# Performance work log

Measured on AMD Instinct MI355X. Metric: run time of the kernel, lower is better.

The kernel has to match this reference:

```python
import jax, jax.numpy as jnp
import numpy as np

E, D, H, K, CH = 32, 512, 512, 4, 32  # n_sources, input_dim, hidden_dim, sparse_topk, confidence hidden
B = 2048
EPS = 1e-6

def setup_inputs() -> dict:
    key = jax.random.key(0)
    ks = jax.random.split(key, 8)
    init = lambda k, shape, fan_in: (jax.random.normal(k, shape, jnp.float32) / np.sqrt(fan_in)).astype(jnp.float32)
    return {
        "x":   jax.random.normal(ks[0], (B, D), jnp.float32),
        # per-expert transform MLPs (stacked over experts)
        "W1":  init(ks[1], (E, D, H), D), "b1": jnp.zeros((E, H), jnp.float32),
        "W2":  init(ks[2], (E, H, D), H), "b2": jnp.zeros((E, D), jnp.float32),
        # gating network
        "Wg1": init(ks[3], (D, H), D),    "bg1": jnp.zeros((H,), jnp.float32),
        "Wg2": init(ks[4], (H, E), H),    "bg2": jnp.zeros((E,), jnp.float32),
        # per-expert confidence nets
        "Wc1": init(ks[5], (E, D, CH), D), "bc1": jnp.zeros((E, CH), jnp.float32),
        "Wc2": init(ks[6], (E, CH, 1), CH), "bc2": jnp.zeros((E, 1), jnp.float32),
    }

def reference(x, W1, b1, W2, b2, Wg1, bg1, Wg2, bg2, Wc1, bc1, Wc2, bc2):
    # gate: softmax over experts, then top-k selection per token
    logits = jax.nn.relu(x @ Wg1 + bg1) @ Wg2 + bg2          # [B, E]
    weights = jax.nn.softmax(logits, axis=-1)                # [B, E]
    _, topi = jax.lax.top_k(weights, K)                      # [B, K] distinct expert ids

    # scan over experts, accumulating weighted-sum numerator and denominator.
    # out = sum_sel (w*c*o) / (sum_sel (w*c) + eps)  ==  torch's normalize-then-combine.
    def body(carry, packed):
        num, den = carry
        w1, bb1, w2, bb2, wc1, bbc1, wc2, bbc2, e = packed
        o = jax.nn.relu(x @ w1 + bb1) @ w2 + bb2             # [B, D] expert output
        c = jax.nn.sigmoid(jax.nn.relu(o @ wc1 + bbc1) @ wc2 + bbc2)[:, 0]  # [B]
        sel = jnp.any(topi == e, axis=1)                     # [B] token routed to expert e?
        cw = weights[:, e] * sel.astype(x.dtype) * c         # [B] gate-weight * confidence
        return (num + cw[:, None] * o, den + cw), None

    init = (jnp.zeros_like(x), jnp.zeros((x.shape[0],), x.dtype))
    (num, den), _ = jax.lax.scan(
        body, init,
        (W1, b1, W2, b2, Wc1, bc1, Wc2, bc2, jnp.arange(E, dtype=topi.dtype)))
    out = num / (den[:, None] + EPS)                         # [B, D]
    return out
```

## Files before the change

kernel.cpp:

```cpp
#include <hip/hip_runtime.h>
#include <hip/hip_bf16.h>

#define BT 2048
#define DD 512
#define HH 512
#define EE 32
#define KK 4
#define CHN 32
#define MAXCH 160

#define NB_CVT 512
#define NB_TRWC 272
#define NB_TRW 2112
#define NB_PREP (NB_CVT + NB_TRWC + NB_TRW)

typedef unsigned int u32;
typedef unsigned short u16;
typedef __attribute__((ext_vector_type(8))) short short8;
typedef __attribute__((ext_vector_type(4))) float f32x4;
typedef __attribute__((ext_vector_type(2))) u32 u32x2;
typedef __attribute__((ext_vector_type(4))) u32 u32x4;

__device__ inline u16 f2bf(float f) {
  u32 u = __builtin_bit_cast(u32, f);
  u32 r = (u + 0x7FFFu + ((u >> 16) & 1u)) >> 16;
  return (u16)r;
}
__device__ inline float bf16f(u16 b) {
  u32 u = ((u32)b) << 16;
  return __builtin_bit_cast(float, u);
}
__device__ inline u32 pack2bf(float a, float b) {
  return (u32)f2bf(a) | ((u32)f2bf(b) << 16);
}
__device__ inline void gload_lds16(const u32* g, u32* l) {
  __builtin_amdgcn_global_load_lds((const __attribute__((address_space(1))) u32*)g,
                                   (__attribute__((address_space(3))) u32*)l, 16, 0, 0);
}

__global__ __launch_bounds__(256)
void k_prep(const float* __restrict__ x, const float* __restrict__ W1,
            const float* __restrict__ W2, const float* __restrict__ Wc1,
            const float* __restrict__ Wg1, const float* __restrict__ Wg2,
            u16* __restrict__ xh, u16* __restrict__ xl,
            u32* __restrict__ img, u32* __restrict__ img_c) {
  const int bx = blockIdx.x;
  const int tid = threadIdx.x;
  if (bx < NB_CVT) {
    int gid = bx * 256 + tid;
    const float4* src = reinterpret_cast<const float4*>(x) + (size_t)gid * 2;
    float4 a = src[0], b = src[1];
    u32x4 hi = { pack2bf(a.x, a.y), pack2bf(a.z, a.w),
                 pack2bf(b.x, b.y), pack2bf(b.z, b.w) };
    float lx0 = a.x - bf16f(f2bf(a.x)), lx1 = a.y - bf16f(f2bf(a.y));
    float lx2 = a.z - bf16f(f2bf(a.z)), lx3 = a.w - bf16f(f2bf(a.w));
    float lx4 = b.x - bf16f(f2bf(b.x)), lx5 = b.y - bf16f(f2bf(b.y));
    float lx6 = b.z - bf16f(f2bf(b.z)), lx7 = b.w - bf16f(f2bf(b.w));
    u32x4 lo = { pack2bf(lx0, lx1), pack2bf(lx2, lx3),
                 pack2bf(lx4, lx5), pack2bf(lx6, lx7) };
    reinterpret_cast<u32x4*>(xh)[gid] = hi;
    reinterpret_cast<u32x4*>(xl)[gid] = lo;
  } else if (bx < NB_CVT + NB_TRWC) {
    int idx = (bx - NB_CVT) * 2 + (tid >> 7);
    int e = idx >> 4, s = idx & 15;
    int t127 = tid & 127;
    int q = t127 >> 5, col = t127 & 31;
    const float* W = (e < EE) ? (Wc1 + (size_t)e * DD * CHN) : Wg2;
    float v[8];
#pragma unroll
    for (int j = 0; j < 8; ++j)
      v[j] = W[(size_t)(s * 32 + q * 8 + j) * CHN + col];
    if (e == 33) {
#pragma unroll
      for (int j = 0; j < 8; ++j)
        v[j] = v[j] - bf16f(f2bf(v[j]));
    }
    u32x4 fr = { pack2bf(v[0], v[1]), pack2bf(v[2], v[3]),
                 pack2bf(v[4], v[5]), pack2bf(v[6], v[7]) };
    *reinterpret_cast<u32x4*>(img_c + ((size_t)e * 16 + s) * 512 + q * 128 + col * 4) = fr;
  } else {
    int u = bx - (NB_CVT + NB_TRWC);
    int z = u >> 5;
    int s = (u >> 1) & 15;
    int n = (u & 1) * 256 + tid;
    const float* W = (z < EE) ? (W1 + (size_t)z * DD * HH)
                   : (z < 2 * EE) ? (W2 + (size_t)(z - EE) * HH * DD)
                   : Wg1;
    float v[32];
#pragma unroll
    for (int k = 0; k < 32; k++)
      v[k] = W[(size_t)(s * 32 + k) * 512 + n];
    if (z == 65) {
#pragma unroll
      for (int k = 0; k < 32; k++)
        v[k] = v[k] - bf16f(f2bf(v[k]));
    }
    int nc = n >> 7, coll = n & 127;
    u32* ob = img + ((size_t)(z * 4 + nc) * 16 + s) * 2048 + coll * 4;
#pragma unroll
    for (int g = 0; g < 4; g++) {
      u32x4 fr = { pack2bf(v[g * 8 + 0], v[g * 8 + 1]),
                   pack2bf(v[g * 8 + 2], v[g * 8 + 3]),
                   pack2bf(v[g * 8 + 4], v[g * 8 + 5]),
                   pack2bf(v[g * 8 + 6], v[g * 8 + 7]) };
      *reinterpret_cast<u32x4*>(ob + g * 512) = fr;
    }
  }
}

__global__ __launch_bounds__(256)
void k_gate_mfma(const u16* __restrict__ xh, const u16* __restrict__ xl,
                 const u32* __restrict__ img, const float* __restrict__ bg1,
                 u16* __restrict__ hh, u16* __restrict__ hl) {
  __shared__ u32 stg[2][2][1024];
  const int chunk = blockIdx.x;
  const int hc = blockIdx.y;
  const int tid = threadIdx.x;
  const int w = tid >> 6, lane = tid & 63;
  const int l15 = lane & 15, q = lane >> 4;
  const int wm = w & 1, wn = w >> 1;
  const int nc = hc >> 1, co = (hc & 1) * 64;
  const u32* imgh = img + ((size_t)(64 * 4 + nc) * 16) * 2048;
  const u32* imgl = img + ((size_t)(65 * 4 + nc) * 16) * 2048;
  const int sq = tid >> 6, scol = tid & 63;
  auto stage = [&](int s, int b) {
    gload_lds16(imgh + s * 2048 + sq * 512 + (co + scol) * 4, stg[b][0] + tid * 4);
    gload_lds16(imgl + s * 2048 + sq * 512 + (co + scol) * 4, stg[b][1] + tid * 4);
  };
  const int t0 = chunk * 64 + wn * 32 + l15;
  const int t1 = t0 + 16;
  auto ldb = [&](const u16* src, int t, int s) {
    return *reinterpret_cast<const short8*>(src + (size_t)t * 512 + s * 32 + q * 8);
  };

  f32x4 acc[2][2];
#pragma unroll
  for (int a = 0; a < 2; a++)
#pragma unroll
    for (int b = 0; b < 2; b++) acc[a][b] = {0.f, 0.f, 0.f, 0.f};

  stage(0, 0);
  short8 bh[2], bl[2];
  bh[0] = ldb(xh, t0, 0); bh[1] = ldb(xh, t1, 0);
  bl[0] = ldb(xl, t0, 0); bl[1] = ldb(xl, t1, 0);
  __syncthreads();

  for (int s = 0; s < 16; ++s) {
    const u32* ch = stg[s & 1][0];
    const u32* cl = stg[s & 1][1];
    short8 nh[2], nl[2];
    if (s < 15) {
      stage(s + 1, (s + 1) & 1);
      nh[0] = ldb(xh, t0, s + 1); nh[1] = ldb(xh, t1, s + 1);
      nl[0] = ldb(xl, t0, s + 1); nl[1] = ldb(xl, t1, s + 1);
    }
#pragma unroll
    for (int mf = 0; mf < 2; ++mf) {
      int col = wm * 32 + mf * 16 + l15;
      short8 ah = *reinterpret_cast<const short8*>(ch + q * 256 + col * 4);
      short8 al = *reinterpret_cast<const short8*>(cl + q * 256 + col * 4);
#pragma unroll
      for (int nf = 0; nf < 2; ++nf) {
        acc[mf][nf] = __builtin_amdgcn_mfma_f32_16x16x32_bf16(ah, bh[nf], acc[mf][nf], 0, 0, 0);
        acc[mf][nf] = __builtin_amdgcn_mfma_f32_16x16x32_bf16(ah, bl[nf], acc[mf][nf], 0, 0, 0);
        acc[mf][nf] = __builtin_amdgcn_mfma_f32_16x16x32_bf16(al, bh[nf], acc[mf][nf], 0, 0, 0);
        acc[mf][nf] = __builtin_amdgcn_mfma_f32_16x16x32_bf16(al, bl[nf], acc[mf][nf], 0, 0, 0);
      }
    }
    __syncthreads();
    if (s < 15) {
      bh[0] = nh[0]; bh[1] = nh[1];
      bl[0] = nl[0]; bl[1] = nl[1];
    }
  }

#pragma unroll
  for (int mf = 0; mf < 2; ++mf) {
    int hcol = hc * 64 + wm * 32 + mf * 16 + q * 4;
    float4 bb = *reinterpret_cast<const float4*>(&bg1[hcol]);
#pragma unroll
    for (int nf = 0; nf < 2; ++nf) {
      int t = chunk * 64 + wn * 32 + nf * 16 + l15;
      float v0 = fmaxf(acc[mf][nf].x + bb.x, 0.f);
      float v1 = fmaxf(acc[mf][nf].y + bb.y, 0.f);
      float v2 = fmaxf(acc[mf][nf].z + bb.z, 0.f);
      float v3 = fmaxf(acc[mf][nf].w + bb.w, 0.f);
      u32x2 hi = { pack2bf(v0, v1), pack2bf(v2, v3) };
      float r0 = v0 - bf16f(f2bf(v0)), r1 = v1 - bf16f(f2bf(v1));
      float r2 = v2 - bf16f(f2bf(v2)), r3 = v3 - bf16f(f2bf(v3));
      u32x2 lo = { pack2bf(r0, r1), pack2bf(r2, r3) };
      *reinterpret_cast<u32x2*>(hh + (size_t)t * 512 + hcol) = hi;
      *reinterpret_cast<u32x2*>(hl + (size_t)t * 512 + hcol) = lo;
    }
  }
}

__global__ __launch_bounds__(256)
void k_route2(const u16* __restrict__ hh, const u16* __restrict__ hl,
              const u32* __restrict__ img_c, const float* __restrict__ bg2,
              float* __restrict__ wts, int* __restrict__ topi) {
  __shared__ u32 sh[8192];
  __shared__ u32 sl_[8192];
  const int chunk = blockIdx.x;
  const int tid = threadIdx.x;
  const int w = tid >> 6, lane = tid & 63;
  const int l15 = lane & 15, q = lane >> 4;
  const u32* srch = img_c + (size_t)32 * 16 * 512;
  const u32* srcl = img_c + (size_t)33 * 16 * 512;
#pragma unroll
  for (int i = 0; i < 8; ++i) {
    gload_lds16(srch + tid * 4 + i * 1024, sh + tid * 4 + i * 1024);
    gload_lds16(srcl + tid * 4 + i * 1024, sl_ + tid * 4 + i * 1024);
  }
  __syncthreads();

  const int t = chunk * 64 + w * 16 + l15;
  const u16* rh = hh + (size_t)t * 512;
  const u16* rl = hl + (size_t)t * 512;
  f32x4 acc0 = {0.f, 0.f, 0.f, 0.f}, acc1 = {0.f, 0.f, 0.f, 0.f};
#pragma unroll
  for (int st = 0; st < 16; ++st) {
    short8 bh = *reinterpret_cast<const short8*>(rh + st * 32 + q * 8);
    short8 bl = *reinterpret_cast<const short8*>(rl + st * 32 + q * 8);
    short8 ah0 = *reinterpret_cast<const short8*>(sh + st * 512 + q * 128 + l15 * 4);
    short8 ah1 = *reinterpret_cast<const short8*>(sh + st * 512 + q * 128 + (16 + l15) * 4);
    short8 al0 = *reinterpret_cast<const short8*>(sl_ + st * 512 + q * 128 + l15 * 4);
    short8 al1 = *reinterpret_cast<const short8*>(sl_ + st * 512 + q * 128 + (16 + l15) * 4);
    acc0 = __builtin_amdgcn_mfma_f32_16x16x32_bf16(ah0, bh, acc0, 0, 0, 0);
    acc0 = __builtin_amdgcn_mfma_f32_16x16x32_bf16(ah0, bl, acc0, 0, 0, 0);
    acc0 = __builtin_amdgcn_mfma_f32_16x16x32_bf16(al0, bh, acc0, 0, 0, 0);
    acc0 = __builtin_amdgcn_mfma_f32_16x16x32_bf16(al0, bl, acc0, 0, 0, 0);
    acc1 = __builtin_amdgcn_mfma_f32_16x16x32_bf16(ah1, bh, acc1, 0, 0, 0);
    acc1 = __builtin_amdgcn_mfma_f32_16x16x32_bf16(ah1, bl, acc1, 0, 0, 0);
    acc1 = __builtin_amdgcn_mfma_f32_16x16x32_bf16(al1, bh, acc1, 0, 0, 0);
    acc1 = __builtin_amdgcn_mfma_f32_16x16x32_bf16(al1, bl, acc1, 0, 0, 0);
  }

  float lv[8];
  int li[8];
#pragma unroll
  for (int i = 0; i < 4; ++i) {
    li[i] = q * 4 + i;
    lv[i] = acc0[i] + bg2[li[i]];
    li[4 + i] = 16 + q * 4 + i;
    lv[4 + i] = acc1[i] + bg2[li[4 + i]];
  }
  float mx = lv[0];
#pragma unroll
  for (int k = 1; k < 8; ++k) mx = fmaxf(mx, lv[k]);
  mx = fmaxf(mx, __shfl_xor(mx, 16));
  mx = fmaxf(mx, __shfl_xor(mx, 32));
  float ex[8], sm = 0.f;
#pragma unroll
  for (int k = 0; k < 8; ++k) { ex[k] = expf(lv[k] - mx); sm += ex[k]; }
  sm += __shfl_xor(sm, 16);
  sm += __shfl_xor(sm, 32);
  float inv = 1.f / sm;
  float4 w0 = { ex[0] * inv, ex[1] * inv, ex[2] * inv, ex[3] * inv };
  float4 w1 = { ex[4] * inv, ex[5] * inv, ex[6] * inv, ex[7] * inv };
  *reinterpret_cast<float4*>(&wts[(size_t)t * EE + q * 4]) = w0;
  *reinterpret_cast<float4*>(&wts[(size_t)t * EE + 16 + q * 4]) = w1;
  unsigned used = 0;
  for (int j = 0; j < KK; ++j) {
    float bv = -1e30f;
    int bi = 64;
#pragma unroll
    for (int k = 0; k < 8; ++k) {
      if (!((used >> k) & 1u) && (lv[k] > bv || (lv[k] == bv && li[k] < bi))) {
        bv = lv[k]; bi = li[k];
      }
    }
#pragma unroll
    for (int m = 16; m <= 32; m <<= 1) {
      float ov = __shfl_xor(bv, m);
      int oi = __shfl_xor(bi, m);
      if (ov > bv || (ov == bv && oi < bi)) { bv = ov; bi = oi; }
    }
    if (q == 0) topi[(t << 2) | j] = bi;
#pragma unroll
    for (int k = 0; k < 8; ++k)
      if (li[k] == bi) used |= 1u << k;
  }
}

__global__ __launch_bounds__(1024)
void k_build(const int* __restrict__ topi, int* __restrict__ cnt,
             int* __restrict__ tlist, int* __restrict__ chunk2e,
             int* __restrict__ chunkloc) {
  __shared__ int lcnt[EE];
  const int tid = threadIdx.x;
  if (tid < EE) lcnt[tid] = 0;
  __syncthreads();
  for (int i = tid; i < BT * KK; i += 1024) {
    int e = topi[i];
    int pos = atomicAdd(&lcnt[e], 1);
    tlist[(size_t)e * BT + pos] = i;
  }
  __syncthreads();
  if (tid < EE) {
    int e = tid;
    cnt[e] = lcnt[e];
    int off = 0, tot = 0;
    for (int j = 0; j < EE; ++j) {
      int nj = (lcnt[j] + 63) >> 6;
      if (j < e) off += nj;
      tot += nj;
    }
    int myn = (lcnt[e] + 63) >> 6;
    for (int j = 0; j < myn; ++j) {
      chunk2e[off + j] = e; chunkloc[off + j] = j;
    }
    for (int idx = tot + e; idx < MAXCH; idx += EE) {
      chunk2e[idx] = -1; chunkloc[idx] = 0;
    }
  }
}

__device__ inline int remap_chunk(int bx) {
  return (bx & 7) * (MAXCH / 8) + (bx >> 3);
}

__global__ __launch_bounds__(256)
void k_gemm1(const u16* __restrict__ xb, const u32* __restrict__ img,
             const float* __restrict__ b1, const int* __restrict__ cnt,
             const int* __restrict__ tlist, const int* __restrict__ chunk2e,
             const int* __restrict__ chunkloc, u32* __restrict__ hid) {
  __shared__ u32 stg[2][4096];
  __shared__ int tkl[64];
  const int c = remap_chunk(blockIdx.x);
  const int e = chunk2e[c];
  if (e < 0) return;
  const int hc = blockIdx.y;
  const int loc = chunkloc[c];
  const int nt = cnt[e];
  const int tid = threadIdx.x;
  const int w = tid >> 6, lane = tid & 63;
  const int l15 = lane & 15, q = lane >> 4;
  const int wm = w & 1, wn = w >> 1;

  const u32* imgb = img + ((size_t)(e * 4 + hc) * 16) * 2048;
  auto stage = [&](int st, u32* dst) {
    const u32* src = imgb + st * 4096;
#pragma unroll
    for (int i = 0; i < 4; i++)
      gload_lds16(src + tid * 4 + i * 1024, dst + tid * 4 + i * 1024);
  };

  stage(0, stg[0]);
  if (tid < 64) {
    int i = min(loc * 64 + tid, nt - 1);
    tkl[tid] = tlist[(size_t)e * BT + i] >> 2;
  }
  __syncthreads();

  const int t0 = tkl[wn * 32 + l15];
  const int t1 = tkl[wn * 32 + 16 + l15];
  auto ldb = [&](int t, int st, int ss) {
    return *reinterpret_cast<const short8*>(
        xb + (size_t)t * 512 + st * 64 + ss * 32 + q * 8);
  };

  f32x4 acc[4][2];
#pragma unroll
  for (int a = 0; a < 4; a++)
#pragma unroll
    for (int b = 0; b < 2; b++) acc[a][b] = {0.f, 0.f, 0.f, 0.f};

  short8 bfr[2][2];
  bfr[0][0] = ldb(t0, 0, 0); bfr[0][1] = ldb(t0, 0, 1);
  bfr[1][0] = ldb(t1, 0, 0); bfr[1][1] = ldb(t1, 0, 1);

  for (int st = 0; st < 8; ++st) {
    const u32* cur = stg[st & 1];
    short8 nb[2][2];
    if (st < 7) {
      stage(st + 1, stg[(st + 1) & 1]);
      nb[0][0] = ldb(t0, st + 1, 0); nb[0][1] = ldb(t0, st + 1, 1);
      nb[1][0] = ldb(t1, st + 1, 0); nb[1][1] = ldb(t1, st + 1, 1);
    }
#pragma unroll
    for (int ss = 0; ss < 2; ++ss) {
#pragma unroll
      for (int mf = 0; mf < 4; ++mf) {
        int col = wm * 64 + mf * 16 + l15;
        short8 af = *reinterpret_cast<const short8*>(
            cur + ss * 2048 + q * 512 + col * 4);
        acc[mf][0] = __builtin_amdgcn_mfma_f32_16x16x32_bf16(af, bfr[0][ss], acc[mf][0], 0, 0, 0);
        acc[mf][1] = __builtin_amdgcn_mfma_f32_16x16x32_bf16(af, bfr[1][ss], acc[mf][1], 0, 0, 0);
      }
    }
    __syncthreads();
    if (st < 7) {
      bfr[0][0] = nb[0][0]; bfr[0][1] = nb[0][1];
      bfr[1][0] = nb[1][0]; bfr[1][1] = nb[1][1];
    }
  }

  const float* b1e = b1 + (size_t)e * HH;
#pragma unroll
  for (int mf = 0; mf < 4; ++mf) {
    int h0 = hc * 128 + wm * 64 + mf * 16 + q * 4;
    float4 bb = *reinterpret_cast<const float4*>(b1e + h0);
#pragma unroll
    for (int nf = 0; nf < 2; ++nf) {
      int local = wn * 32 + nf * 16 + l15;
      int prow = c * 64 + local;
      float v0 = fmaxf(acc[mf][nf].x + bb.x, 0.f);
      float v1 = fmaxf(acc[mf][nf].y + bb.y, 0.f);
      float v2 = fmaxf(acc[mf][nf].z + bb.z, 0.f);
      float v3 = fmaxf(acc[mf][nf].w + bb.w, 0.f);
      u32x2 pk = { pack2bf(v0, v1), pack2bf(v2, v3) };
      *reinterpret_cast<u32x2*>(hid + (size_t)prow * 256 + (h0 >> 1)) = pk;
    }
  }
}

__global__ __launch_bounds__(256)
void k_gemm2(const u32* __restrict__ hid, const u32* __restrict__ img,
             const float* __restrict__ b2, const int* __restrict__ cnt,
             const int* __restrict__ tlist, const int* __restrict__ chunk2e,
             const int* __restrict__ chunkloc, u16* __restrict__ o_p) {
  __shared__ u32 stg[2][4096];
  __shared__ int tke[64];
  const int c = remap_chunk(blockIdx.x);
  const int e = chunk2e[c];
  if (e < 0) return;
  const int dc = blockIdx.y;
  const int loc = chunkloc[c];
  const int nt = cnt[e];
  const int tid = threadIdx.x;
  const int w = tid >> 6, lane = tid & 63;
  const int l15 = lane & 15, q = lane >> 4;
  const int wm = w & 1, wn = w >> 1;
  const int rows_c = min(64, nt - loc * 64);

  const u32* imgb = img + ((size_t)((EE + e) * 4 + dc) * 16) * 2048;
  auto stage = [&](int st, u32* dst) {
    const u32* src = imgb + st * 4096;
#pragma unroll
    for (int i = 0; i < 4; i++)
      gload_lds16(src + tid * 4 + i * 1024, dst + tid * 4 + i * 1024);
  };

  stage(0, stg[0]);
  if (tid < 64) {
    int i = min(loc * 64 + tid, nt - 1);
    tke[tid] = tlist[(size_t)e * BT + i];
  }
  __syncthreads();

  const u16* hid16 = (const u16*)hid;
  const int pr0 = c * 64 + wn * 32 + l15;
  const int pr1 = pr0 + 16;
  auto ldb = [&](int pr, int st, int ss) {
    return *reinterpret_cast<const short8*>(
        hid16 + (size_t)pr * 512 + st * 64 + ss * 32 + q * 8);
  };

  f32x4 acc[4][2];
#pragma unroll
  for (int a = 0; a < 4; a++)
#pragma unroll
    for (int b = 0; b < 2; b++) acc[a][b] = {0.f, 0.f, 0.f, 0.f};

  short8 bfr[2][2];
  bfr[0][0] = ldb(pr0, 0, 0); bfr[0][1] = ldb(pr0, 0, 1);
  bfr[1][0] = ldb(pr1, 0, 0); bfr[1][1] = ldb(pr1, 0, 1);

  for (int st = 0; st < 8; ++st) {
    const u32* cur = stg[st & 1];
    short8 nb[2][2];
    if (st < 7) {
      stage(st + 1, stg[(st + 1) & 1]);
      nb[0][0] = ldb(pr0, st + 1, 0); nb[0][1] = ldb(pr0, st + 1, 1);
      nb[1][0] = ldb(pr1, st + 1, 0); nb[1][1] = ldb(pr1, st + 1, 1);
    }
#pragma unroll
    for (int ss = 0; ss < 2; ++ss) {
#pragma unroll
      for (int mf = 0; mf < 4; ++mf) {
        int col = wm * 64 + mf * 16 + l15;
        short8 af = *reinterpret_cast<const short8*>(
            cur + ss * 2048 + q * 512 + col * 4);
        acc[mf][0] = __builtin_amdgcn_mfma_f32_16x16x32_bf16(af, bfr[0][ss], acc[mf][0], 0, 0, 0);
        acc[mf][1] = __builtin_amdgcn_mfma_f32_16x16x32_bf16(af, bfr[1][ss], acc[mf][1], 0, 0, 0);
      }
    }
    __syncthreads();
    if (st < 7) {
      bfr[0][0] = nb[0][0]; bfr[0][1] = nb[0][1];
      bfr[1][0] = nb[1][0]; bfr[1][1] = nb[1][1];
    }
  }

  const float* b2e = b2 + (size_t)e * DD;
#pragma unroll
  for (int mf = 0; mf < 4; ++mf) {
    int d0 = dc * 128 + wm * 64 + mf * 16 + q * 4;
    float4 bb = *reinterpret_cast<const float4*>(b2e + d0);
#pragma unroll
    for (int nf = 0; nf < 2; ++nf) {
      int local = wn * 32 + nf * 16 + l15;
      if (local < rows_c) {
        int ent = tke[local];
        u32x2 pk = { pack2bf(acc[mf][nf].x + bb.x, acc[mf][nf].y + bb.y),
                     pack2bf(acc[mf][nf].z + bb.z, acc[mf][nf].w + bb.w) };
        *reinterpret_cast<u32x2*>(&o_p[(size_t)ent * DD + d0]) = pk;
      }
    }
  }
}

__global__ __launch_bounds__(256)
void k_conf2(const u16* __restrict__ o_p, const u32* __restrict__ img_c,
             const float* __restrict__ bc1, const float* __restrict__ Wc2,
             const float* __restrict__ bc2, const float* __restrict__ wts,
             const int* __restrict__ cnt, const int* __restrict__ tlist,
             const int* __restrict__ chunk2e, const int* __restrict__ chunkloc,
             float* __restrict__ cw) {
  __shared__ u32 stg[8192];
  __shared__ int tke[64];
  const int c = remap_chunk(blockIdx.x);
  const int e = chunk2e[c];
  if (e < 0) return;
  const int loc = chunkloc[c];
  const int nt = cnt[e];
  const int tid = threadIdx.x;
  const int w = tid >> 6, lane = tid & 63;
  const int l15 = lane & 15, q = lane >> 4;

  const u32* src = img_c + (size_t)e * 16 * 512;
#pragma unroll
  for (int i = 0; i < 8; ++i)
    gload_lds16(src + tid * 4 + i * 1024, stg + tid * 4 + i * 1024);
  if (tid < 64) {
    int i = min(loc * 64 + tid, nt - 1);
    tke[tid] = tlist[(size_t)e * BT + i];
  }
  __syncthreads();

  const int rows_c = min(64, nt - loc * 64);
  const int local = w * 16 + l15;
  const int ent = tke[local];
  const u16* orow = o_p + (size_t)ent * DD;

  f32x4 acc0 = {0.f, 0.f, 0.f, 0.f}, acc1 = {0.f, 0.f, 0.f, 0.f};
#pragma unroll
  for (int st = 0; st < 16; ++st) {
    short8 bfrag = *reinterpret_cast<const short8*>(orow + st * 32 + q * 8);
    short8 af0 = *reinterpret_cast<const short8*>(
        stg + st * 512 + q * 128 + l15 * 4);
    short8 af1 = *reinterpret_cast<const short8*>(
        stg + st * 512 + q * 128 + (16 + l15) * 4);
    acc0 = __builtin_amdgcn_mfma_f32_16x16x32_bf16(af0, bfrag, acc0, 0, 0, 0);
    acc1 = __builtin_amdgcn_mfma_f32_16x16x32_bf16(af1, bfrag, acc1, 0, 0, 0);
  }

  float part = 0.f;
#pragma unroll
  for (int i = 0; i < 4; ++i) {
    int ch0 = q * 4 + i, ch1 = 16 + q * 4 + i;
    float h0 = fmaxf(acc0[i] + bc1[(size_t)e * CHN + ch0], 0.f);
    float h1 = fmaxf(acc1[i] + bc1[(size_t)e * CHN + ch1], 0.f);
    part = fmaf(h0, Wc2[(size_t)e * CHN + ch0], part);
    part = fmaf(h1, Wc2[(size_t)e * CHN + ch1], part);
  }
  part += __shfl_xor(part, 16);
  part += __shfl_xor(part, 32);
  if (q == 0 && local < rows_c) {
    float cv = 1.f / (1.f + expf(-(part + bc2[e])));
    cw[ent] = wts[(size_t)(ent >> 2) * EE + e] * cv;
  }
}

__global__ __launch_bounds__(256)
void k_combine(const u16* __restrict__ o_p, const float* __restrict__ cw,
               float* __restrict__ out) {
  int gid = blockIdx.x * 256 + threadIdx.x;
  int t = gid >> 6;
  int j = gid & 63;
  float c0 = cw[t * 4 + 0], c1 = cw[t * 4 + 1];
  float c2 = cw[t * 4 + 2], c3 = cw[t * 4 + 3];
  float den = c0 + c1 + c2 + c3 + 1e-6f;
  const u16* base = o_p + (size_t)t * 4 * DD + j * 8;
  short8 v0 = *reinterpret_cast<const short8*>(base + 0 * DD);
  short8 v1 = *reinterpret_cast<const short8*>(base + 1 * DD);
  short8 v2 = *reinterpret_cast<const short8*>(base + 2 * DD);
  short8 v3 = *reinterpret_cast<const short8*>(base + 3 * DD);
  float r[8];
#pragma unroll
  for (int i = 0; i < 8; ++i) {
    r[i] = (c0 * bf16f((u16)v0[i]) + c1 * bf16f((u16)v1[i]) +
            c2 * bf16f((u16)v2[i]) + c3 * bf16f((u16)v3[i])) / den;
  }
  float4 o0 = { r[0], r[1], r[2], r[3] };
  float4 o1 = { r[4], r[5], r[6], r[7] };
  float4* dst = reinterpret_cast<float4*>(out + (size_t)t * DD + j * 8);
  dst[0] = o0;
  dst[1] = o1;
}

extern "C" void kernel_launch(void* const* d_in, const int* in_sizes, int n_in,
                              void* d_out, int out_size, void* d_ws, size_t ws_size,
                              hipStream_t stream) {
  const float* x   = (const float*)d_in[0];
  const float* W1  = (const float*)d_in[1];
  const float* b1  = (const float*)d_in[2];
  const float* W2  = (const float*)d_in[3];
  const float* b2  = (const float*)d_in[4];
  const float* Wg1 = (const float*)d_in[5];
  const float* bg1 = (const float*)d_in[6];
  const float* Wg2 = (const float*)d_in[7];
  const float* bg2 = (const float*)d_in[8];
  const float* Wc1 = (const float*)d_in[9];
  const float* bc1 = (const float*)d_in[10];
  const float* Wc2 = (const float*)d_in[11];
  const float* bc2 = (const float*)d_in[12];
  float* out = (float*)d_out;

  char* p = (char*)d_ws;
  u16* xh = (u16*)p;            p += (size_t)BT * DD * 2;
  u32* img = (u32*)p;           p += (size_t)66 * 4 * 16 * 2048 * 4;
  u16* hh = (u16*)p;
  u16* hl = (u16*)(p + (size_t)2 * 1024 * 1024);
  u16* xl = (u16*)(p + (size_t)4 * 1024 * 1024);
  u32* hid = (u32*)p;           p += (size_t)MAXCH * 64 * DD * 2;
  float* wts = (float*)p;       p += (size_t)BT * EE * 4;
  float* cw  = (float*)p;       p += (size_t)BT * KK * 4;
  u16* o_p = (u16*)p;           p += (size_t)BT * KK * DD * 2;
  int* cnt = (int*)p;           p += 256;
  int* tlist = (int*)p;         p += (size_t)EE * BT * 4;
  int* chunk2e = (int*)p;       p += 1024;
  int* chunkloc = (int*)p;      p += 1024;
  u32* img_c = (u32*)p;         p += (size_t)34 * 16 * 512 * 4;
  int* topi = (int*)p;          p += (size_t)BT * KK * 4;

  k_prep<<<NB_PREP, 256, 0, stream>>>(x, W1, W2, Wc1, Wg1, Wg2,
                                      xh, xl, img, img_c);
  k_gate_mfma<<<dim3(32, 8), 256, 0, stream>>>(xh, xl, img, bg1, hh, hl);
  k_route2<<<32, 256, 0, stream>>>(hh, hl, img_c, bg2, wts, topi);
  k_build<<<1, 1024, 0, stream>>>(topi, cnt, tlist, chunk2e, chunkloc);
  k_gemm1<<<dim3(MAXCH, 4), 256, 0, stream>>>(xh, img, b1, cnt, tlist,
                                              chunk2e, chunkloc, hid);
  k_gemm2<<<dim3(MAXCH, 4), 256, 0, stream>>>(hid, img, b2, cnt, tlist,
                                              chunk2e, chunkloc, o_p);
  k_conf2<<<MAXCH, 256, 0, stream>>>(o_p, img_c, bc1, Wc2, bc2, wts,
                                     cnt, tlist, chunk2e, chunkloc, cw);
  k_combine<<<(BT * (DD / 8)) / 256, 256, 0, stream>>>(o_p, cw, out);
}
```

Measured before the change: 103.3 us.

## Fuse gate, route and build kernels, and conf into gemm2, via last-block atomics

Merges the gate GEMM, the routing softmax/top-k and the expert list build into one kernel. The last block to finish each token chunk does the routing, and the last block overall builds the per-expert token lists, both detected with atomic counters and thread fences. In the same way, the confidence net is folded into gemm2: the last of the four column blocks per chunk computes it. This removes three kernel launches and their inter-kernel gaps, at the cost of serialized tail work in single blocks, an extra memset of the flag counters, and a larger shared-memory footprint.

```diff
diff --git a/kernel.cpp b/kernel.cpp
--- a/kernel.cpp
+++ b/kernel.cpp
@@ -109,209 +109,220 @@
 }
 
 __global__ __launch_bounds__(256)
-void k_gate_mfma(const u16* __restrict__ xh, const u16* __restrict__ xl,
-                 const u32* __restrict__ img, const float* __restrict__ bg1,
-                 u16* __restrict__ hh, u16* __restrict__ hl) {
-  __shared__ u32 stg[2][2][1024];
+void k_gate_fused(const u16* __restrict__ xh, const u16* __restrict__ xl,
+                  const u32* __restrict__ img, const float* __restrict__ bg1,
+                  const u32* __restrict__ img_c, const float* __restrict__ bg2,
+                  u16* __restrict__ hh, u16* __restrict__ hl,
+                  float* __restrict__ wts, int* __restrict__ topi,
+                  int* __restrict__ done1, int* __restrict__ gdone,
+                  int* __restrict__ cnt, int* __restrict__ tlist,
+                  int* __restrict__ chunk2e, int* __restrict__ chunkloc) {
+  __shared__ u32 smem[16384];
+  __shared__ int winflag, bwin;
   const int chunk = blockIdx.x;
   const int hc = blockIdx.y;
   const int tid = threadIdx.x;
   const int w = tid >> 6, lane = tid & 63;
   const int l15 = lane & 15, q = lane >> 4;
   const int wm = w & 1, wn = w >> 1;
-  const int nc = hc >> 1, co = (hc & 1) * 64;
-  const u32* imgh = img + ((size_t)(64 * 4 + nc) * 16) * 2048;
-  const u32* imgl = img + ((size_t)(65 * 4 + nc) * 16) * 2048;
-  const int sq = tid >> 6, scol = tid & 63;
-  auto stage = [&](int s, int b) {
-    gload_lds16(imgh + s * 2048 + sq * 512 + (co + scol) * 4, stg[b][0] + tid * 4);
-    gload_lds16(imgl + s * 2048 + sq * 512 + (co + scol) * 4, stg[b][1] + tid * 4);
-  };
-  const int t0 = chunk * 64 + wn * 32 + l15;
-  const int t1 = t0 + 16;
-  auto ldb = [&](const u16* src, int t, int s) {
-    return *reinterpret_cast<const short8*>(src + (size_t)t * 512 + s * 32 + q * 8);
-  };
-
-  f32x4 acc[2][2];
-#pragma unroll
-  for (int a = 0; a < 2; a++)
-#pragma unroll
-    for (int b = 0; b < 2; b++) acc[a][b] = {0.f, 0.f, 0.f, 0.f};
-
-  stage(0, 0);
-  short8 bh[2], bl[2];
-  bh[0] = ldb(xh, t0, 0); bh[1] = ldb(xh, t1, 0);
-  bl[0] = ldb(xl, t0, 0); bl[1] = ldb(xl, t1, 0);
+
+  {
+    auto S = [&](int b, int h2) { return smem + (b * 2 + h2) * 1024; };
+    const int nc = hc >> 1, co = (hc & 1) * 64;
+    const u32* imgh = img + ((size_t)(64 * 4 + nc) * 16) * 2048;
+    const u32* imgl = img + ((size_t)(65 * 4 + nc) * 16) * 2048;
+    const int sq = tid >> 6, scol = tid & 63;
+    auto stage = [&](int s, int b) {
+      gload_lds16(imgh + s * 2048 + sq * 512 + (co + scol) * 4, S(b, 0) + tid * 4);
+      gload_lds16(imgl + s * 2048 + sq * 512 + (co + scol) * 4, S(b, 1) + tid * 4);
+    };
+    const int t0 = chunk * 64 + wn * 32 + l15;
+    const int t1 = t0 + 16;
+    auto ldb = [&](const u16* src, int t, int s) {
+      return *reinterpret_cast<const short8*>(src + (size_t)t * 512 + s * 32 + q * 8);
+    };
+
+    f32x4 acc[2][2];
+#pragma unroll
+    for (int a = 0; a < 2; a++)
+#pragma unroll
+      for (int b = 0; b < 2; b++) acc[a][b] = {0.f, 0.f, 0.f, 0.f};
+
+    stage(0, 0);
+    short8 bh[2], bl[2];
+    bh[0] = ldb(xh, t0, 0); bh[1] = ldb(xh, t1, 0);
+    bl[0] = ldb(xl, t0, 0); bl[1] = ldb(xl, t1, 0);
+    __syncthreads();
+
+    for (int s = 0; s < 16; ++s) {
+      const u32* ch = S(s & 1, 0);
+      const u32* cl = S(s & 1, 1);
+      short8 nh[2], nl[2];
+      if (s < 15) {
+        stage(s + 1, (s + 1) & 1);
+        nh[0] = ldb(xh, t0, s + 1); nh[1] = ldb(xh, t1, s + 1);
+        nl[0] = ldb(xl, t0, s + 1); nl[1] = ldb(xl, t1, s + 1);
+      }
+#pragma unroll
+      for (int mf = 0; mf < 2; ++mf) {
+        int col = wm * 32 + mf * 16 + l15;
+        short8 ah = *reinterpret_cast<const short8*>(ch + q * 256 + col * 4);
+        short8 al = *reinterpret_cast<const short8*>(cl + q * 256 + col * 4);
+#pragma unroll
+        for (int nf = 0; nf < 2; ++nf) {
+          acc[mf][nf] = __builtin_amdgcn_mfma_f32_16x16x32_bf16(ah, bh[nf], acc[mf][nf], 0, 0, 0);
+          acc[mf][nf] = __builtin_amdgcn_mfma_f32_16x16x32_bf16(ah, bl[nf], acc[mf][nf], 0, 0, 0);
+          acc[mf][nf] = __builtin_amdgcn_mfma_f32_16x16x32_bf16(al, bh[nf], acc[mf][nf], 0, 0, 0);
+          acc[mf][nf] = __builtin_amdgcn_mfma_f32_16x16x32_bf16(al, bl[nf], acc[mf][nf], 0, 0, 0);
+        }
+      }
+      __syncthreads();
+      if (s < 15) {
+        bh[0] = nh[0]; bh[1] = nh[1];
+        bl[0] = nl[0]; bl[1] = nl[1];
+      }
+    }
+
+#pragma unroll
+    for (int mf = 0; mf < 2; ++mf) {
+      int hcol = hc * 64 + wm * 32 + mf * 16 + q * 4;
+      float4 bb = *reinterpret_cast<const float4*>(&bg1[hcol]);
+#pragma unroll
+      for (int nf = 0; nf < 2; ++nf) {
+        int t = chunk * 64 + wn * 32 + nf * 16 + l15;
+        float v0 = fmaxf(acc[mf][nf].x + bb.x, 0.f);
+        float v1 = fmaxf(acc[mf][nf].y + bb.y, 0.f);
+        float v2 = fmaxf(acc[mf][nf].z + bb.z, 0.f);
+        float v3 = fmaxf(acc[mf][nf].w + bb.w, 0.f);
+        u32x2 hi = { pack2bf(v0, v1), pack2bf(v2, v3) };
+        float r0 = v0 - bf16f(f2bf(v0)), r1 = v1 - bf16f(f2bf(v1));
+        float r2 = v2 - bf16f(f2bf(v2)), r3 = v3 - bf16f(f2bf(v3));
+        u32x2 lo = { pack2bf(r0, r1), pack2bf(r2, r3) };
+        *reinterpret_cast<u32x2*>(hh + (size_t)t * 512 + hcol) = hi;
+        *reinterpret_cast<u32x2*>(hl + (size_t)t * 512 + hcol) = lo;
+      }
+    }
+  }
+
+  __threadfence();
+  if (tid == 0) winflag = (atomicAdd(&done1[chunk], 1) == 7);
   __syncthreads();
-
-  for (int s = 0; s < 16; ++s) {
-    const u32* ch = stg[s & 1][0];
-    const u32* cl = stg[s & 1][1];
-    short8 nh[2], nl[2];
-    if (s < 15) {
-      stage(s + 1, (s + 1) & 1);
-      nh[0] = ldb(xh, t0, s + 1); nh[1] = ldb(xh, t1, s + 1);
-      nl[0] = ldb(xl, t0, s + 1); nl[1] = ldb(xl, t1, s + 1);
-    }
-#pragma unroll
-    for (int mf = 0; mf < 2; ++mf) {
-      int col = wm * 32 + mf * 16 + l15;
-      short8 ah = *reinterpret_cast<const short8*>(ch + q * 256 + col * 4);
-      short8 al = *reinterpret_cast<const short8*>(cl + q * 256 + col * 4);
-#pragma unroll
-      for (int nf = 0; nf < 2; ++nf) {
-        acc[mf][nf] = __builtin_amdgcn_mfma_f32_16x16x32_bf16(ah, bh[nf], acc[mf][nf], 0, 0, 0);
-        acc[mf][nf] = __builtin_amdgcn_mfma_f32_16x16x32_bf16(ah, bl[nf], acc[mf][nf], 0, 0, 0);
-        acc[mf][nf] = __builtin_amdgcn_mfma_f32_16x16x32_bf16(al, bh[nf], acc[mf][nf], 0, 0, 0);
-        acc[mf][nf] = __builtin_amdgcn_mfma_f32_16x16x32_bf16(al, bl[nf], acc[mf][nf], 0, 0, 0);
-      }
+  if (!winflag) return;
+  __threadfence();
+
+  {
+    u32* sh = smem;
+    u32* sl_ = smem + 8192;
+    const u32* srch = img_c + (size_t)32 * 16 * 512;
+    const u32* srcl = img_c + (size_t)33 * 16 * 512;
+#pragma unroll
+    for (int i = 0; i < 8; ++i) {
+      gload_lds16(srch + tid * 4 + i * 1024, sh + tid * 4 + i * 1024);
+      gload_lds16(srcl + tid * 4 + i * 1024, sl_ + tid * 4 + i * 1024);
     }
     __syncthreads();
-    if (s < 15) {
-      bh[0] = nh[0]; bh[1] = nh[1];
-      bl[0] = nl[0]; bl[1] = nl[1];
-    }
-  }
-
-#pragma unroll
-  for (int mf = 0; mf < 2; ++mf) {
-    int hcol = hc * 64 + wm * 32 + mf * 16 + q * 4;
-    float4 bb = *reinterpret_cast<const float4*>(&bg1[hcol]);
-#pragma unroll
-    for (int nf = 0; nf < 2; ++nf) {
-      int t = chunk * 64 + wn * 32 + nf * 16 + l15;
-      float v0 = fmaxf(acc[mf][nf].x + bb.x, 0.f);
-      float v1 = fmaxf(acc[mf][nf].y + bb.y, 0.f);
-      float v2 = fmaxf(acc[mf][nf].z + bb.z, 0.f);
-      float v3 = fmaxf(acc[mf][nf].w + bb.w, 0.f);
-      u32x2 hi = { pack2bf(v0, v1), pack2bf(v2, v3) };
-      float r0 = v0 - bf16f(f2bf(v0)), r1 = v1 - bf16f(f2bf(v1));
-      float r2 = v2 - bf16f(f2bf(v2)), r3 = v3 - bf16f(f2bf(v3));
-      u32x2 lo = { pack2bf(r0, r1), pack2bf(r2, r3) };
-      *reinterpret_cast<u32x2*>(hh + (size_t)t * 512 + hcol) = hi;
-      *reinterpret_cast<u32x2*>(hl + (size_t)t * 512 + hcol) = lo;
-    }
-  }
-}
-
-__global__ __launch_bounds__(256)
-void k_route2(const u16* __restrict__ hh, const u16* __restrict__ hl,
-              const u32* __restrict__ img_c, const float* __restrict__ bg2,
-              float* __restrict__ wts, int* __restrict__ topi) {
-  __shared__ u32 sh[8192];
-  __shared__ u32 sl_[8192];
-  const int chunk = blockIdx.x;
-  const int tid = threadIdx.x;
-  const int w = tid >> 6, lane = tid & 63;
-  const int l15 = lane & 15, q = lane >> 4;
-  const u32* srch = img_c + (size_t)32 * 16 * 512;
-  const u32* srcl = img_c + (size_t)33 * 16 * 512;
-#pragma unroll
-  for (int i = 0; i < 8; ++i) {
-    gload_lds16(srch + tid * 4 + i * 1024, sh + tid * 4 + i * 1024);
-    gload_lds16(srcl + tid * 4 + i * 1024, sl_ + tid * 4 + i * 1024);
-  }
+
+    const int t = chunk * 64 + w * 16 + l15;
+    const u16* rh = hh + (size_t)t * 512;
+    const u16* rl = hl + (size_t)t * 512;
+    f32x4 acc0 = {0.f, 0.f, 0.f, 0.f}, acc1 = {0.f, 0.f, 0.f, 0.f};
+#pragma unroll
+    for (int st = 0; st < 16; ++st) {
+      short8 bh = *reinterpret_cast<const short8*>(rh + st * 32 + q * 8);
+      short8 bl = *reinterpret_cast<const short8*>(rl + st * 32 + q * 8);
+      short8 ah0 = *reinterpret_cast<const short8*>(sh + st * 512 + q * 128 + l15 * 4);
+      short8 ah1 = *reinterpret_cast<const short8*>(sh + st * 512 + q * 128 + (16 + l15) * 4);
+      short8 al0 = *reinterpret_cast<const short8*>(sl_ + st * 512 + q * 128 + l15 * 4);
+      short8 al1 = *reinterpret_cast<const short8*>(sl_ + st * 512 + q * 128 + (16 + l15) * 4);
+      acc0 = __builtin_amdgcn_mfma_f32_16x16x32_bf16(ah0, bh, acc0, 0, 0, 0);
+      acc0 = __builtin_amdgcn_mfma_f32_16x16x32_bf16(ah0, bl, acc0, 0, 0, 0);
+      acc0 = __builtin_amdgcn_mfma_f32_16x16x32_bf16(al0, bh, acc0, 0, 0, 0);
+      acc0 = __builtin_amdgcn_mfma_f32_16x16x32_bf16(al0, bl, acc0, 0, 0, 0);
+      acc1 = __builtin_amdgcn_mfma_f32_16x16x32_bf16(ah1, bh, acc1, 0, 0, 0);
+      acc1 = __builtin_amdgcn_mfma_f32_16x16x32_bf16(ah1, bl, acc1, 0, 0, 0);
+      acc1 = __builtin_amdgcn_mfma_f32_16x16x32_bf16(al1, bh, acc1, 0, 0, 0);
+      acc1 = __builtin_amdgcn_mfma_f32_16x16x32_bf16(al1, bl, acc1, 0, 0, 0);
+    }
+
+    float lv[8];
+    int li[8];
+#pragma unroll
+    for (int i = 0; i < 4; ++i) {
+      li[i] = q * 4 + i;
+      lv[i] = acc0[i] + bg2[li[i]];
+      li[4 + i] = 16 + q * 4 + i;
+      lv[4 + i] = acc1[i] + bg2[li[4 + i]];
+    }
+    float mx = lv[0];
+#pragma unroll
+    for (int k = 1; k < 8; ++k) mx = fmaxf(mx, lv[k]);
+    mx = fmaxf(mx, __shfl_xor(mx, 16));
+    mx = fmaxf(mx, __shfl_xor(mx, 32));
+    float ex[8], sm = 0.f;
+#pragma unroll
+    for (int k = 0; k < 8; ++k) { ex[k] = expf(lv[k] - mx); sm += ex[k]; }
+    sm += __shfl_xor(sm, 16);
+    sm += __shfl_xor(sm, 32);
+    float inv = 1.f / sm;
+    float4 w0 = { ex[0] * inv, ex[1] * inv, ex[2] * inv, ex[3] * inv };
+    float4 w1 = { ex[4] * inv, ex[5] * inv, ex[6] * inv, ex[7] * inv };
+    *reinterpret_cast<float4*>(&wts[(size_t)t * EE + q * 4]) = w0;
+    *reinterpret_cast<float4*>(&wts[(size_t)t * EE + 16 + q * 4]) = w1;
+    unsigned used = 0;
+    for (int j = 0; j < KK; ++j) {
+      float bv = -1e30f;
+      int bi = 64;
+#pragma unroll
+      for (int k = 0; k < 8; ++k) {
+        if (!((used >> k) & 1u) && (lv[k] > bv || (lv[k] == bv && li[k] < bi))) {
+          bv = lv[k]; bi = li[k];
+        }
+      }
+#pragma unroll
+      for (int m = 16; m <= 32; m <<= 1) {
+        float ov = __shfl_xor(bv, m);
+        int oi = __shfl_xor(bi, m);
+        if (ov > bv || (ov == bv && oi < bi)) { bv = ov; bi = oi; }
+      }
+      if (q == 0) topi[(t << 2) | j] = bi;
+#pragma unroll
+      for (int k = 0; k < 8; ++k)
+        if (li[k] == bi) used |= 1u << k;
+    }
+  }
+
+  __threadfence();
+  if (tid == 0) bwin = (atomicAdd(gdone, 1) == 31);
   __syncthreads();
-
-  const int t = chunk * 64 + w * 16 + l15;
-  const u16* rh = hh + (size_t)t * 512;
-  const u16* rl = hl + (size_t)t * 512;
-  f32x4 acc0 = {0.f, 0.f, 0.f, 0.f}, acc1 = {0.f, 0.f, 0.f, 0.f};
-#pragma unroll
-  for (int st = 0; st < 16; ++st) {
-    short8 bh = *reinterpret_cast<const short8*>(rh + st * 32 + q * 8);
-    short8 bl = *reinterpret_cast<const short8*>(rl + st * 32 + q * 8);
-    short8 ah0 = *reinterpret_cast<const short8*>(sh + st * 512 + q * 128 + l15 * 4);
-    short8 ah1 = *reinterpret_cast<const short8*>(sh + st * 512 + q * 128 + (16 + l15) * 4);
-    short8 al0 = *reinterpret_cast<const short8*>(sl_ + st * 512 + q * 128 + l15 * 4);
-    short8 al1 = *reinterpret_cast<const short8*>(sl_ + st * 512 + q * 128 + (16 + l15) * 4);
-    acc0 = __builtin_amdgcn_mfma_f32_16x16x32_bf16(ah0, bh, acc0, 0, 0, 0);
-    acc0 = __builtin_amdgcn_mfma_f32_16x16x32_bf16(ah0, bl, acc0, 0, 0, 0);
-    acc0 = __builtin_amdgcn_mfma_f32_16x16x32_bf16(al0, bh, acc0, 0, 0, 0);
-    acc0 = __builtin_amdgcn_mfma_f32_16x16x32_bf16(al0, bl, acc0, 0, 0, 0);
-    acc1 = __builtin_amdgcn_mfma_f32_16x16x32_bf16(ah1, bh, acc1, 0, 0, 0);
-    acc1 = __builtin_amdgcn_mfma_f32_16x16x32_bf16(ah1, bl, acc1, 0, 0, 0);
-    acc1 = __builtin_amdgcn_mfma_f32_16x16x32_bf16(al1, bh, acc1, 0, 0, 0);
-    acc1 = __builtin_amdgcn_mfma_f32_16x16x32_bf16(al1, bl, acc1, 0, 0, 0);
-  }
-
-  float lv[8];
-  int li[8];
-#pragma unroll
-  for (int i = 0; i < 4; ++i) {
-    li[i] = q * 4 + i;
-    lv[i] = acc0[i] + bg2[li[i]];
-    li[4 + i] = 16 + q * 4 + i;
-    lv[4 + i] = acc1[i] + bg2[li[4 + i]];
-  }
-  float mx = lv[0];
-#pragma unroll
-  for (int k = 1; k < 8; ++k) mx = fmaxf(mx, lv[k]);
-  mx = fmaxf(mx, __shfl_xor(mx, 16));
-  mx = fmaxf(mx, __shfl_xor(mx, 32));
-  float ex[8], sm = 0.f;
-#pragma unroll
-  for (int k = 0; k < 8; ++k) { ex[k] = expf(lv[k] - mx); sm += ex[k]; }
-  sm += __shfl_xor(sm, 16);
-  sm += __shfl_xor(sm, 32);
-  float inv = 1.f / sm;
-  float4 w0 = { ex[0] * inv, ex[1] * inv, ex[2] * inv, ex[3] * inv };
-  float4 w1 = { ex[4] * inv, ex[5] * inv, ex[6] * inv, ex[7] * inv };
-  *reinterpret_cast<float4*>(&wts[(size_t)t * EE + q * 4]) = w0;
-  *reinterpret_cast<float4*>(&wts[(size_t)t * EE + 16 + q * 4]) = w1;
-  unsigned used = 0;
-  for (int j = 0; j < KK; ++j) {
-    float bv = -1e30f;
-    int bi = 64;
-#pragma unroll
-    for (int k = 0; k < 8; ++k) {
-      if (!((used >> k) & 1u) && (lv[k] > bv || (lv[k] == bv && li[k] < bi))) {
-        bv = lv[k]; bi = li[k];
-      }
-    }
-#pragma unroll
-    for (int m = 16; m <= 32; m <<= 1) {
-      float ov = __shfl_xor(bv, m);
-      int oi = __shfl_xor(bi, m);
-      if (ov > bv || (ov == bv && oi < bi)) { bv = ov; bi = oi; }
-    }
-    if (q == 0) topi[(t << 2) | j] = bi;
-#pragma unroll
-    for (int k = 0; k < 8; ++k)
-      if (li[k] == bi) used |= 1u << k;
-  }
-}
-
-__global__ __launch_bounds__(1024)
-void k_build(const int* __restrict__ topi, int* __restrict__ cnt,
-             int* __restrict__ tlist, int* __restrict__ chunk2e,
-             int* __restrict__ chunkloc) {
-  __shared__ int lcnt[EE];
-  const int tid = threadIdx.x;
-  if (tid < EE) lcnt[tid] = 0;
-  __syncthreads();
-  for (int i = tid; i < BT * KK; i += 1024) {
-    int e = topi[i];
-    int pos = atomicAdd(&lcnt[e], 1);
-    tlist[(size_t)e * BT + pos] = i;
-  }
-  __syncthreads();
-  if (tid < EE) {
-    int e = tid;
-    cnt[e] = lcnt[e];
-    int off = 0, tot = 0;
-    for (int j = 0; j < EE; ++j) {
-      int nj = (lcnt[j] + 63) >> 6;
-      if (j < e) off += nj;
-      tot += nj;
-    }
-    int myn = (lcnt[e] + 63) >> 6;
-    for (int j = 0; j < myn; ++j) {
-      chunk2e[off + j] = e; chunkloc[off + j] = j;
-    }
-    for (int idx = tot + e; idx < MAXCH; idx += EE) {
-      chunk2e[idx] = -1; chunkloc[idx] = 0;
+  if (!bwin) return;
+  __threadfence();
+
+  {
+    int* lcnt = (int*)smem;
+    if (tid < EE) lcnt[tid] = 0;
+    __syncthreads();
+    for (int i = tid; i < BT * KK; i += 256) {
+      int e2 = topi[i];
+      int pos = atomicAdd(&lcnt[e2], 1);
+      tlist[(size_t)e2 * BT + pos] = i;
+    }
+    __syncthreads();
+    if (tid < EE) {
+      int e2 = tid;
+      cnt[e2] = lcnt[e2];
+      int off = 0, tot = 0;
+      for (int j = 0; j < EE; ++j) {
+        int nj = (lcnt[j] + 63) >> 6;
+        if (j < e2) off += nj;
+        tot += nj;
+      }
+      int myn = (lcnt[e2] + 63) >> 6;
+      for (int j = 0; j < myn; ++j) {
+        chunk2e[off + j] = e2; chunkloc[off + j] = j;
+      }
+      for (int idx = tot + e2; idx < MAXCH; idx += EE) {
+        chunk2e[idx] = -1; chunkloc[idx] = 0;
+      }
     }
   }
 }
@@ -416,12 +427,17 @@
 }
 
 __global__ __launch_bounds__(256)
-void k_gemm2(const u32* __restrict__ hid, const u32* __restrict__ img,
-             const float* __restrict__ b2, const int* __restrict__ cnt,
-             const int* __restrict__ tlist, const int* __restrict__ chunk2e,
-             const int* __restrict__ chunkloc, u16* __restrict__ o_p) {
+void k_gemm2c(const u32* __restrict__ hid, const u32* __restrict__ img,
+              const float* __restrict__ b2, const int* __restrict__ cnt,
+              const int* __restrict__ tlist, const int* __restrict__ chunk2e,
+              const int* __restrict__ chunkloc, u16* __restrict__ o_p,
+              const u32* __restrict__ img_c, const float* __restrict__ bc1,
+              const float* __restrict__ Wc2, const float* __restrict__ bc2,
+              const float* __restrict__ wts, int* __restrict__ done2,
+              float* __restrict__ cw) {
   __shared__ u32 stg[2][4096];
   __shared__ int tke[64];
+  __shared__ int cwin;
   const int c = remap_chunk(blockIdx.x);
   const int e = chunk2e[c];
   if (e < 0) return;
@@ -509,67 +525,52 @@
       }
     }
   }
-}
-
-__global__ __launch_bounds__(256)
-void k_conf2(const u16* __restrict__ o_p, const u32* __restrict__ img_c,
-             const float* __restrict__ bc1, const float* __restrict__ Wc2,
-             const float* __restrict__ bc2, const float* __restrict__ wts,
-             const int* __restrict__ cnt, const int* __restrict__ tlist,
-             const int* __restrict__ chunk2e, const int* __restrict__ chunkloc,
-             float* __restrict__ cw) {
-  __shared__ u32 stg[8192];
-  __shared__ int tke[64];
-  const int c = remap_chunk(blockIdx.x);
-  const int e = chunk2e[c];
-  if (e < 0) return;
-  const int loc = chunkloc[c];
-  const int nt = cnt[e];
-  const int tid = threadIdx.x;
-  const int w = tid >> 6, lane = tid & 63;
-  const int l15 = lane & 15, q = lane >> 4;
-
-  const u32* src = img_c + (size_t)e * 16 * 512;
-#pragma unroll
-  for (int i = 0; i < 8; ++i)
-    gload_lds16(src + tid * 4 + i * 1024, stg + tid * 4 + i * 1024);
-  if (tid < 64) {
-    int i = min(loc * 64 + tid, nt - 1);
-    tke[tid] = tlist[(size_t)e * BT + i];
-  }
+
+  __threadfence();
+  if (tid == 0) cwin = (atomicAdd(&done2[c], 1) == 3);
   __syncthreads();
-
-  const int rows_c = min(64, nt - loc * 64);
-  const int local = w * 16 + l15;
-  const int ent = tke[local];
-  const u16* orow = o_p + (size_t)ent * DD;
-
-  f32x4 acc0 = {0.f, 0.f, 0.f, 0.f}, acc1 = {0.f, 0.f, 0.f, 0.f};
-#pragma unroll
-  for (int st = 0; st < 16; ++st) {
-    short8 bfrag = *reinterpret_cast<const short8*>(orow + st * 32 + q * 8);
-    short8 af0 = *reinterpret_cast<const short8*>(
-        stg + st * 512 + q * 128 + l15 * 4);
-    short8 af1 = *reinterpret_cast<const short8*>(
-        stg + st * 512 + q * 128 + (16 + l15) * 4);
-    acc0 = __builtin_amdgcn_mfma_f32_16x16x32_bf16(af0, bfrag, acc0, 0, 0, 0);
-    acc1 = __builtin_amdgcn_mfma_f32_16x16x32_bf16(af1, bfrag, acc1, 0, 0, 0);
-  }
-
-  float part = 0.f;
-#pragma unroll
-  for (int i = 0; i < 4; ++i) {
-    int ch0 = q * 4 + i, ch1 = 16 + q * 4 + i;
-    float h0 = fmaxf(acc0[i] + bc1[(size_t)e * CHN + ch0], 0.f);
-    float h1 = fmaxf(acc1[i] + bc1[(size_t)e * CHN + ch1], 0.f);
-    part = fmaf(h0, Wc2[(size_t)e * CHN + ch0], part);
-    part = fmaf(h1, Wc2[(size_t)e * CHN + ch1], part);
-  }
-  part += __shfl_xor(part, 16);
-  part += __shfl_xor(part, 32);
-  if (q == 0 && local < rows_c) {
-    float cv = 1.f / (1.f + expf(-(part + bc2[e])));
-    cw[ent] = wts[(size_t)(ent >> 2) * EE + e] * cv;
+  if (!cwin) return;
+  __threadfence();
+
+  {
+    u32* cs = &stg[0][0];
+    const u32* src = img_c + (size_t)e * 16 * 512;
+#pragma unroll
+    for (int i = 0; i < 8; ++i)
+      gload_lds16(src + tid * 4 + i * 1024, cs + tid * 4 + i * 1024);
+    __syncthreads();
+
+    const int local = w * 16 + l15;
+    const int ent = tke[local];
+    const u16* orow = o_p + (size_t)ent * DD;
+
+    f32x4 acc0 = {0.f, 0.f, 0.f, 0.f}, acc1 = {0.f, 0.f, 0.f, 0.f};
+#pragma unroll
+    for (int st = 0; st < 16; ++st) {
+      short8 bfrag = *reinterpret_cast<const short8*>(orow + st * 32 + q * 8);
+      short8 af0 = *reinterpret_cast<const short8*>(
+          cs + st * 512 + q * 128 + l15 * 4);
+      short8 af1 = *reinterpret_cast<const short8*>(
+          cs + st * 512 + q * 128 + (16 + l15) * 4);
+      acc0 = __builtin_amdgcn_mfma_f32_16x16x32_bf16(af0, bfrag, acc0, 0, 0, 0);
+      acc1 = __builtin_amdgcn_mfma_f32_16x16x32_bf16(af1, bfrag, acc1, 0, 0, 0);
+    }
+
+    float part = 0.f;
+#pragma unroll
+    for (int i = 0; i < 4; ++i) {
+      int ch0 = q * 4 + i, ch1 = 16 + q * 4 + i;
+      float h0 = fmaxf(acc0[i] + bc1[(size_t)e * CHN + ch0], 0.f);
+      float h1 = fmaxf(acc1[i] + bc1[(size_t)e * CHN + ch1], 0.f);
+      part = fmaf(h0, Wc2[(size_t)e * CHN + ch0], part);
+      part = fmaf(h1, Wc2[(size_t)e * CHN + ch1], part);
+    }
+    part += __shfl_xor(part, 16);
+    part += __shfl_xor(part, 32);
+    if (q == 0 && local < rows_c) {
+      float cv = 1.f / (1.f + expf(-(part + bc2[e])));
+      cw[ent] = wts[(size_t)(ent >> 2) * EE + e] * cv;
+    }
   }
 }
 
@@ -634,17 +635,22 @@
   int* chunkloc = (int*)p;      p += 1024;
   u32* img_c = (u32*)p;         p += (size_t)34 * 16 * 512 * 4;
   int* topi = (int*)p;          p += (size_t)BT * KK * 4;
-
+  int* flags = (int*)p;         p += 1024;
+  int* done1 = flags;
+  int* gdone = flags + 32;
+  int* done2 = flags + 33;
+
+  hipMemsetAsync(flags, 0, 1024, stream);
   k_prep<<<NB_PREP, 256, 0, stream>>>(x, W1, W2, Wc1, Wg1, Wg2,
                                       xh, xl, img, img_c);
-  k_gate_mfma<<<dim3(32, 8), 256, 0, stream>>>(xh, xl, img, bg1, hh, hl);
-  k_route2<<<32, 256, 0, stream>>>(hh, hl, img_c, bg2, wts, topi);
-  k_build<<<1, 1024, 0, stream>>>(topi, cnt, tlist, chunk2e, chunkloc);
+  k_gate_fused<<<dim3(32, 8), 256, 0, stream>>>(xh, xl, img, bg1, img_c, bg2,
+                                                hh, hl, wts, topi, done1, gdone,
+                                                cnt, tlist, chunk2e, chunkloc);
   k_gemm1<<<dim3(MAXCH, 4), 256, 0, stream>>>(xh, img, b1, cnt, tlist,
                                               chunk2e, chunkloc, hid);
-  k_gemm2<<<dim3(MAXCH, 4), 256, 0, stream>>>(hid, img, b2, cnt, tlist,
-                                              chunk2e, chunkloc, o_p);
-  k_conf2<<<MAXCH, 256, 0, stream>>>(o_p, img_c, bc1, Wc2, bc2, wts,
-                                     cnt, tlist, chunk2e, chunkloc, cw);
+  k_gemm2c<<<dim3(MAXCH, 4), 256, 0, stream>>>(hid, img, b2, cnt, tlist,
+                                               chunk2e, chunkloc, o_p,
+                                               img_c, bc1, Wc2, bc2, wts,
+                                               done2, cw);
   k_combine<<<(BT * (DD / 8)) / 256, 256, 0, stream>>>(o_p, cw, out);
 }
```

After: 226.3 us. +119.1%, slower.
